# Kernel optimization log

Measured on AMD Instinct MI355X. Metric: run time of the kernel, lower is better.

The kernel has to match this reference:

```python
import jax, jax.numpy as jnp
import numpy as np

N_LEVELS = 16
F_PER_LEVEL = 2
LOG2_T = 19
TABLE_SIZE = 1 << LOG2_T
BASE_RES = 16.0
FINEST_RES = 512.0
# W == H == 512 -> x1 = y1 = 1.0
BOX_MIN = jnp.array([-1.0, -1.0], dtype=jnp.float32)
BOX_MAX = jnp.array([1.0, 1.0], dtype=jnp.float32)
# corner offsets, same order as torch BOX_OFFSETS: (0,0),(0,1),(1,0),(1,1)
OFFSETS = jnp.array([[i, j] for i in (0, 1) for j in (0, 1)], dtype=jnp.int32)
PRIME0 = jnp.uint32(1)
PRIME1 = jnp.uint32(2654435761)
HASH_MASK = jnp.uint32(TABLE_SIZE - 1)


def setup_inputs() -> dict:
    key = jax.random.key(0)
    ks = jax.random.split(key, 8)
    B, P = 4, 262144
    coord_2D = jax.random.uniform(ks[0], (B, P, 2), dtype=jnp.float32)  # in [0,1) subset of box
    embeddings = jax.random.normal(ks[1], (N_LEVELS, TABLE_SIZE, F_PER_LEVEL), dtype=jnp.float32)
    d_in = 2 + N_LEVELS * F_PER_LEVEL  # 34
    W0 = jax.random.normal(ks[2], (d_in, 256), dtype=jnp.float32) * 0.05
    b0 = jnp.zeros((256,), dtype=jnp.float32)
    W1 = jax.random.normal(ks[3], (256, 256), dtype=jnp.float32) * 0.05
    b1 = jnp.zeros((256,), dtype=jnp.float32)
    W2 = jax.random.normal(ks[4], (256, 3), dtype=jnp.float32) * 0.05
    b2 = jnp.zeros((3,), dtype=jnp.float32)
    return {"coord_2D": coord_2D, "embeddings": embeddings,
            "W0": W0, "b0": b0, "W1": W1, "b1": b1, "W2": W2, "b2": b2}


def _hash(corners_int32):
    # corners: [N,4,2] int32; xor of per-dim prime products, masked to table size (uint32 wraparound semantics)
    c = corners_int32.astype(jnp.uint32)
    h = (c[..., 0] * PRIME0) ^ (c[..., 1] * PRIME1)
    return (h & HASH_MASK).astype(jnp.int32)


def _encode(xy, embeddings):
    # xy: [N,2]; embeddings: [L, T, F]
    b = np.exp((np.log(FINEST_RES) - np.log(BASE_RES)) / (N_LEVELS - 1))
    resolutions = jnp.floor(BASE_RES * (b ** jnp.arange(N_LEVELS, dtype=jnp.float32)))  # [L]

    def level_encode(table, res):
        grid = (BOX_MAX - BOX_MIN) / res                     # [2]
        bl = jnp.floor((xy - BOX_MIN) / grid).astype(jnp.int32)  # bottom-left cell idx [N,2]
        vmin = bl.astype(xy.dtype) * grid + BOX_MIN          # voxel min vertex [N,2]
        w = (xy - vmin) / grid                               # bilinear weights [N,2]
        corners = bl[:, None, :] + OFFSETS                   # [N,4,2]
        emb = table[_hash(corners)]                          # gather: [N,4,F]
        wx = w[:, 0:1]
        wy = w[:, 1:2]
        c00 = emb[:, 0] * (1 - wx) + emb[:, 2] * wx
        c01 = emb[:, 1] * (1 - wx) + emb[:, 3] * wx
        return c00 * (1 - wy) + c01 * wy                     # [N,F]

    enc = jax.vmap(level_encode)(embeddings, resolutions)    # [L,N,F]
    return jnp.moveaxis(enc, 0, 1).reshape(xy.shape[0], N_LEVELS * F_PER_LEVEL)


def reference(coord_2D, embeddings, W0, b0, W1, b1, W2, b2):
    B = coord_2D.shape[0]
    xy = jnp.clip(coord_2D.reshape(-1, 2), BOX_MIN, BOX_MAX)
    enc = _encode(xy, embeddings)
    points_enc = jnp.concatenate([xy, enc], axis=-1)         # [N, 34]
    feat = jax.nn.relu(points_enc @ W0 + b0)
    feat = jax.nn.relu(feat @ W1 + b1)
    rgb = jax.nn.sigmoid(feat @ W2 + b2)
    return rgb.reshape(B, -1, 3)
```

## Files before the change

kernel.cpp:

```cpp
#include <hip/hip_runtime.h>
#include <hip/hip_bf16.h>
#include <cstdint>
#include <cstddef>

#define N_LEVELS   16
#define LOG2_T     19
#define TABLE_SIZE (1u << LOG2_T)
#define HASH_MASK  (TABLE_SIZE - 1u)
#define PRIME1     2654435761u

#define TPB 256
#define BT  64
#define FSTRIDE 72
#define HSTRIDE 264

typedef __attribute__((ext_vector_type(8))) short short8;
typedef __attribute__((ext_vector_type(4))) float floatx4;

__device__ __constant__ float c_res[N_LEVELS] = {
    16.f, 20.f, 25.f, 32.f, 40.f, 50.f, 64.f, 80.f,
    101.f, 128.f, 161.f, 203.f, 256.f, 322.f, 406.f, 512.f
};

__device__ __forceinline__ unsigned short f2bf(float x) {
    union { float f; uint32_t u; } v; v.f = x;
    const uint32_t u = v.u;
    return (unsigned short)((u + 0x7fffu + ((u >> 16) & 1u)) >> 16);
}

__device__ __forceinline__ uint32_t pk_bf16(float a, float b) {
#if __has_builtin(__builtin_amdgcn_cvt_pk_bf16_f32)
    typedef __attribute__((ext_vector_type(2))) __bf16 bf16x2;
    bf16x2 v = __builtin_amdgcn_cvt_pk_bf16_f32(a, b);
    uint32_t u; __builtin_memcpy(&u, &v, 4); return u;
#else
    return (uint32_t)f2bf(a) | ((uint32_t)f2bf(b) << 16);
#endif
}

__global__ void pack_weights(const float* __restrict__ W0,
                             const float* __restrict__ W1,
                             const float* __restrict__ W2,
                             unsigned short* __restrict__ ws)
{
    const int f = blockIdx.x;
    const int lane = threadIdx.x;
    const int q = lane >> 4, r = lane & 15;
    int layer, kt, nt;
    if (f < 32)       { layer = 0; kt = f >> 4;        nt = f & 15; }
    else if (f < 160) { layer = 1; kt = (f - 32) >> 4; nt = (f - 32) & 15; }
    else              { layer = 2; kt = f - 160;       nt = 0; }
    unsigned short vals[8];
    #pragma unroll
    for (int j = 0; j < 8; ++j) {
        const int k = kt * 32 + q * 8 + j;
        const int n = nt * 16 + r;
        float v = 0.f;
        if (layer == 0) {
            if (k < 32)       v = W0[(2 + k) * 256 + n];
            else if (k == 32) v = W0[0 * 256 + n];
            else if (k == 33) v = W0[1 * 256 + n];
        } else if (layer == 1) {
            v = W1[k * 256 + n];
        } else {
            if (n < 3) v = W2[k * 3 + n];
        }
        vals[j] = f2bf(v);
    }
    uint4 pk;
    pk.x = (uint32_t)vals[0] | ((uint32_t)vals[1] << 16);
    pk.y = (uint32_t)vals[2] | ((uint32_t)vals[3] << 16);
    pk.z = (uint32_t)vals[4] | ((uint32_t)vals[5] << 16);
    pk.w = (uint32_t)vals[6] | ((uint32_t)vals[7] << 16);
    *(uint4*)(ws + (size_t)f * 1024 + lane * 8) = pk;
}

__global__ __launch_bounds__(TPB, 2)
void fused_ngp_mlp(const float* __restrict__ coord,
                   const float* __restrict__ emb,
                   const unsigned short* __restrict__ wpack,
                   const float* __restrict__ b0,
                   const float* __restrict__ b1,
                   const float* __restrict__ b2,
                   float* __restrict__ out, int npoints)
{
    __shared__ unsigned short feat[BT][FSTRIDE];
    __shared__ unsigned short h[BT][HSTRIDE];

    const int t = threadIdx.x;
    const int p0 = blockIdx.x * BT;
    const int wave = t >> 6;
    const int lane = t & 63;
    const int q = lane >> 4, r = lane & 15;

    {
        const int p = t >> 2;
        const int k = t & 3;
        const int gp = p0 + p;
        float x = 0.f, y = 0.f;
        if (gp < npoints) {
            x = coord[2 * gp + 0]; y = coord[2 * gp + 1];
            x = fminf(fmaxf(x, -1.f), 1.f);
            y = fminf(fmaxf(y, -1.f), 1.f);
        }
        if (k == 0) {
            feat[p][32] = f2bf(x); feat[p][33] = f2bf(y);
            *(uint32_t*)&feat[p][34] = 0u;
            *(uint32_t*)&feat[p][36] = 0u;
            *(uint32_t*)&feat[p][38] = 0u;
        } else {
            const uint4 z = {0u, 0u, 0u, 0u};
            *(uint4*)&feat[p][40 + 8 * (k - 1)] = z;
        }
        #pragma unroll
        for (int i = 0; i < 4; ++i) {
            const int l = 4 * k + i;
            const float res  = c_res[l];
            const float grid = 2.0f / res;
            const float invg = res * 0.5f;
            const float tx = (x + 1.0f) / grid;
            const float ty = (y + 1.0f) / grid;
            const int bx = (int)floorf(tx);
            const int by = (int)floorf(ty);
            const float vx = (float)bx * grid - 1.0f;
            const float vy = (float)by * grid - 1.0f;
            const float wx = (x - vx) * invg;
            const float wy = (y - vy) * invg;
            const float2* tab = (const float2*)emb + (size_t)l * TABLE_SIZE;
            const uint32_t ux0 = (uint32_t)bx, ux1 = (uint32_t)(bx + 1);
            const uint32_t hy0 = (uint32_t)by * PRIME1;
            const uint32_t hy1 = (uint32_t)(by + 1) * PRIME1;
            const float2 e00 = tab[(ux0 ^ hy0) & HASH_MASK];
            const float2 e01 = tab[(ux0 ^ hy1) & HASH_MASK];
            const float2 e10 = tab[(ux1 ^ hy0) & HASH_MASK];
            const float2 e11 = tab[(ux1 ^ hy1) & HASH_MASK];
            const float owx = 1.f - wx, owy = 1.f - wy;
            const float f0 = (e00.x * owx + e10.x * wx) * owy + (e01.x * owx + e11.x * wx) * wy;
            const float f1 = (e00.y * owx + e10.y * wx) * owy + (e01.y * owx + e11.y * wx) * wy;
            *(uint32_t*)&feat[p][8 * k + 2 * i] = pk_bf16(f0, f1);
        }
    }
    __syncthreads();

    const unsigned short* w0p = wpack;
    const unsigned short* w1p = wpack + 32 * 1024;
    const unsigned short* w2p = wpack + 160 * 1024;

    {
        floatx4 acc[4][4];
        #pragma unroll
        for (int mti = 0; mti < 4; ++mti)
            #pragma unroll
            for (int nt = 0; nt < 4; ++nt)
                acc[mti][nt] = floatx4{0.f, 0.f, 0.f, 0.f};
        #pragma unroll
        for (int kt = 0; kt < 2; ++kt) {
            short8 a[4], b[4];
            #pragma unroll
            for (int mti = 0; mti < 4; ++mti)
                a[mti] = *(const short8*)(w0p + (size_t)(kt * 16 + wave * 4 + mti) * 1024 + lane * 8);
            #pragma unroll
            for (int nt = 0; nt < 4; ++nt)
                b[nt] = *(const short8*)&feat[16 * nt + r][kt * 32 + q * 8];
            #pragma unroll
            for (int mti = 0; mti < 4; ++mti)
                #pragma unroll
                for (int nt = 0; nt < 4; ++nt)
                    acc[mti][nt] = __builtin_amdgcn_mfma_f32_16x16x32_bf16(a[mti], b[nt], acc[mti][nt], 0, 0, 0);
        }
        #pragma unroll
        for (int mti = 0; mti < 4; ++mti) {
            const int col = (wave * 4 + mti) * 16 + 4 * q;
            const float4 bias = *(const float4*)&b0[col];
            #pragma unroll
            for (int nt = 0; nt < 4; ++nt) {
                const floatx4 a = acc[mti][nt];
                uint2 v;
                v.x = pk_bf16(fmaxf(a[0] + bias.x, 0.f), fmaxf(a[1] + bias.y, 0.f));
                v.y = pk_bf16(fmaxf(a[2] + bias.z, 0.f), fmaxf(a[3] + bias.w, 0.f));
                *(uint2*)&h[16 * nt + r][col] = v;
            }
        }
    }
    __syncthreads();

    {
        floatx4 acc[4][4];
        #pragma unroll
        for (int mti = 0; mti < 4; ++mti)
            #pragma unroll
            for (int nt = 0; nt < 4; ++nt)
                acc[mti][nt] = floatx4{0.f, 0.f, 0.f, 0.f};
        #pragma unroll 2
        for (int kt = 0; kt < 8; ++kt) {
            short8 a[4], b[4];
            #pragma unroll
            for (int mti = 0; mti < 4; ++mti)
                a[mti] = *(const short8*)(w1p + (size_t)(kt * 16 + wave * 4 + mti) * 1024 + lane * 8);
            #pragma unroll
            for (int nt = 0; nt < 4; ++nt)
                b[nt] = *(const short8*)&h[16 * nt + r][kt * 32 + q * 8];
            #pragma unroll
            for (int mti = 0; mti < 4; ++mti)
                #pragma unroll
                for (int nt = 0; nt < 4; ++nt)
                    acc[mti][nt] = __builtin_amdgcn_mfma_f32_16x16x32_bf16(a[mti], b[nt], acc[mti][nt], 0, 0, 0);
        }
        __syncthreads();
        #pragma unroll
        for (int mti = 0; mti < 4; ++mti) {
            const int col = (wave * 4 + mti) * 16 + 4 * q;
            const float4 bias = *(const float4*)&b1[col];
            #pragma unroll
            for (int nt = 0; nt < 4; ++nt) {
                const floatx4 a = acc[mti][nt];
                uint2 v;
                v.x = pk_bf16(fmaxf(a[0] + bias.x, 0.f), fmaxf(a[1] + bias.y, 0.f));
                v.y = pk_bf16(fmaxf(a[2] + bias.z, 0.f), fmaxf(a[3] + bias.w, 0.f));
                *(uint2*)&h[16 * nt + r][col] = v;
            }
        }
    }
    __syncthreads();

    {
        floatx4 acc = floatx4{0.f, 0.f, 0.f, 0.f};
        #pragma unroll
        for (int kt = 0; kt < 8; ++kt) {
            const short8 a = *(const short8*)(w2p + (size_t)kt * 1024 + lane * 8);
            const short8 b = *(const short8*)&h[16 * wave + r][kt * 32 + q * 8];
            acc = __builtin_amdgcn_mfma_f32_16x16x32_bf16(a, b, acc, 0, 0, 0);
        }
        if (q == 0) {
            const int gp = p0 + 16 * wave + r;
            if (gp < npoints) {
                #pragma unroll
                for (int reg = 0; reg < 3; ++reg) {
                    const float s = acc[reg] + b2[reg];
                    out[(size_t)gp * 3 + reg] = 1.f / (1.f + expf(-s));
                }
            }
        }
    }
}

extern "C" void kernel_launch(void* const* d_in, const int* in_sizes, int n_in,
                              void* d_out, int out_size, void* d_ws, size_t ws_size,
                              hipStream_t stream) {
    const float* coord = (const float*)d_in[0];
    const float* emb   = (const float*)d_in[1];
    const float* W0    = (const float*)d_in[2];
    const float* b0    = (const float*)d_in[3];
    const float* W1    = (const float*)d_in[4];
    const float* b1    = (const float*)d_in[5];
    const float* W2    = (const float*)d_in[6];
    const float* b2    = (const float*)d_in[7];
    float* out = (float*)d_out;
    unsigned short* ws = (unsigned short*)d_ws;

    const int npoints = in_sizes[0] / 2;
    const int blocks  = (npoints + BT - 1) / BT;

    hipLaunchKernelGGL(pack_weights, dim3(168), dim3(64), 0, stream, W0, W1, W2, ws);
    hipLaunchKernelGGL(fused_ngp_mlp, dim3(blocks), dim3(TPB), 0, stream,
                       coord, emb, ws, b0, b1, b2, out, npoints);
}
```

Baseline: 378.7 us.

## Split hash-grid encoding and MLP into separate kernels via workspace buffer

Replaces the single fused encode+MLP kernel with an encode kernel that writes bf16 features per point to global workspace, followed by an MLP kernel that reads them directly as MFMA B operands. This lets each kernel run with higher occupancy (launch bounds 4 instead of 2) and drops the shared-memory feature staging, so the latency-bound gathers and the MFMA work no longer compete for the same block. In exchange it adds a global round-trip of about 80 bytes per point plus an extra kernel launch. The fused kernel is kept as a fallback when the workspace is too small.

```diff
diff --git a/kernel.cpp b/kernel.cpp
--- a/kernel.cpp
+++ b/kernel.cpp
@@ -11,6 +11,7 @@
 
 #define TPB 256
 #define BT  64
+#define FROW 40
 #define FSTRIDE 72
 #define HSTRIDE 264
 
@@ -75,6 +76,191 @@
     *(uint4*)(ws + (size_t)f * 1024 + lane * 8) = pk;
 }
 
+__global__ __launch_bounds__(TPB, 4)
+void encode_kernel(const float* __restrict__ coord,
+                   const float* __restrict__ emb,
+                   unsigned short* __restrict__ featG, int npoints)
+{
+    const int gp = blockIdx.x * TPB + threadIdx.x;
+    if (gp >= npoints) return;
+    float x = coord[2 * gp + 0];
+    float y = coord[2 * gp + 1];
+    x = fminf(fmaxf(x, -1.f), 1.f);
+    y = fminf(fmaxf(y, -1.f), 1.f);
+
+    uint32_t e[N_LEVELS];
+    #pragma unroll
+    for (int l = 0; l < N_LEVELS; ++l) {
+        const float res  = c_res[l];
+        const float grid = 2.0f / res;
+        const float invg = res * 0.5f;
+        const float tx = (x + 1.0f) / grid;
+        const float ty = (y + 1.0f) / grid;
+        const int bx = (int)floorf(tx);
+        const int by = (int)floorf(ty);
+        const float vx = (float)bx * grid - 1.0f;
+        const float vy = (float)by * grid - 1.0f;
+        const float wx = (x - vx) * invg;
+        const float wy = (y - vy) * invg;
+        const float2* tab = (const float2*)emb + (size_t)l * TABLE_SIZE;
+        const uint32_t ux0 = (uint32_t)bx, ux1 = (uint32_t)(bx + 1);
+        const uint32_t hy0 = (uint32_t)by * PRIME1;
+        const uint32_t hy1 = (uint32_t)(by + 1) * PRIME1;
+        const float2 e00 = tab[(ux0 ^ hy0) & HASH_MASK];
+        const float2 e01 = tab[(ux0 ^ hy1) & HASH_MASK];
+        const float2 e10 = tab[(ux1 ^ hy0) & HASH_MASK];
+        const float2 e11 = tab[(ux1 ^ hy1) & HASH_MASK];
+        const float owx = 1.f - wx, owy = 1.f - wy;
+        const float f0 = (e00.x * owx + e10.x * wx) * owy + (e01.x * owx + e11.x * wx) * wy;
+        const float f1 = (e00.y * owx + e10.y * wx) * owy + (e01.y * owx + e11.y * wx) * wy;
+        e[l] = pk_bf16(f0, f1);
+    }
+
+    unsigned short* row = featG + (size_t)gp * FROW;
+    uint4 v;
+    v.x = e[0];  v.y = e[1];  v.z = e[2];  v.w = e[3];  *(uint4*)(row +  0) = v;
+    v.x = e[4];  v.y = e[5];  v.z = e[6];  v.w = e[7];  *(uint4*)(row +  8) = v;
+    v.x = e[8];  v.y = e[9];  v.z = e[10]; v.w = e[11]; *(uint4*)(row + 16) = v;
+    v.x = e[12]; v.y = e[13]; v.z = e[14]; v.w = e[15]; *(uint4*)(row + 24) = v;
+    v.x = pk_bf16(x, y); v.y = 0u; v.z = 0u; v.w = 0u;  *(uint4*)(row + 32) = v;
+}
+
+__global__ __launch_bounds__(TPB, 4)
+void mlp_kernel(const unsigned short* __restrict__ featG,
+                const unsigned short* __restrict__ wpack,
+                const float* __restrict__ b0,
+                const float* __restrict__ b1,
+                const float* __restrict__ b2,
+                float* __restrict__ out, int npoints)
+{
+    __shared__ unsigned short h[BT][HSTRIDE];
+
+    const int t = threadIdx.x;
+    const int p0 = blockIdx.x * BT;
+    const int wave = t >> 6;
+    const int lane = t & 63;
+    const int q = lane >> 4, r = lane & 15;
+
+    const unsigned short* w0p = wpack;
+    const unsigned short* w1p = wpack + 32 * 1024;
+    const unsigned short* w2p = wpack + 160 * 1024;
+
+    {
+        floatx4 acc[4][4];
+        #pragma unroll
+        for (int mti = 0; mti < 4; ++mti)
+            #pragma unroll
+            for (int nt = 0; nt < 4; ++nt)
+                acc[mti][nt] = floatx4{0.f, 0.f, 0.f, 0.f};
+
+        short8 a[4], b[4];
+        #pragma unroll
+        for (int mti = 0; mti < 4; ++mti)
+            a[mti] = *(const short8*)(w0p + (size_t)(0 * 16 + wave * 4 + mti) * 1024 + lane * 8);
+        #pragma unroll
+        for (int nt = 0; nt < 4; ++nt) {
+            const int row = min(p0 + 16 * nt + r, npoints - 1);
+            b[nt] = *(const short8*)(featG + (size_t)row * FROW + q * 8);
+        }
+        #pragma unroll
+        for (int mti = 0; mti < 4; ++mti)
+            #pragma unroll
+            for (int nt = 0; nt < 4; ++nt)
+                acc[mti][nt] = __builtin_amdgcn_mfma_f32_16x16x32_bf16(a[mti], b[nt], acc[mti][nt], 0, 0, 0);
+        #pragma unroll
+        for (int mti = 0; mti < 4; ++mti)
+            a[mti] = *(const short8*)(w0p + (size_t)(1 * 16 + wave * 4 + mti) * 1024 + lane * 8);
+        #pragma unroll
+        for (int nt = 0; nt < 4; ++nt) {
+            if (q == 0) {
+                const int row = min(p0 + 16 * nt + r, npoints - 1);
+                b[nt] = *(const short8*)(featG + (size_t)row * FROW + 32);
+            } else {
+                b[nt] = short8{0,0,0,0,0,0,0,0};
+            }
+        }
+        #pragma unroll
+        for (int mti = 0; mti < 4; ++mti)
+            #pragma unroll
+            for (int nt = 0; nt < 4; ++nt)
+                acc[mti][nt] = __builtin_amdgcn_mfma_f32_16x16x32_bf16(a[mti], b[nt], acc[mti][nt], 0, 0, 0);
+
+        #pragma unroll
+        for (int mti = 0; mti < 4; ++mti) {
+            const int col = (wave * 4 + mti) * 16 + 4 * q;
+            const float4 bias = *(const float4*)&b0[col];
+            #pragma unroll
+            for (int nt = 0; nt < 4; ++nt) {
+                const floatx4 a4 = acc[mti][nt];
+                uint2 v;
+                v.x = pk_bf16(fmaxf(a4[0] + bias.x, 0.f), fmaxf(a4[1] + bias.y, 0.f));
+                v.y = pk_bf16(fmaxf(a4[2] + bias.z, 0.f), fmaxf(a4[3] + bias.w, 0.f));
+                *(uint2*)&h[16 * nt + r][col] = v;
+            }
+        }
+    }
+    __syncthreads();
+
+    {
+        floatx4 acc[4][4];
+        #pragma unroll
+        for (int mti = 0; mti < 4; ++mti)
+            #pragma unroll
+            for (int nt = 0; nt < 4; ++nt)
+                acc[mti][nt] = floatx4{0.f, 0.f, 0.f, 0.f};
+        #pragma unroll 2
+        for (int kt = 0; kt < 8; ++kt) {
+            short8 a[4], b[4];
+            #pragma unroll
+            for (int mti = 0; mti < 4; ++mti)
+                a[mti] = *(const short8*)(w1p + (size_t)(kt * 16 + wave * 4 + mti) * 1024 + lane * 8);
+            #pragma unroll
+            for (int nt = 0; nt < 4; ++nt)
+                b[nt] = *(const short8*)&h[16 * nt + r][kt * 32 + q * 8];
+            #pragma unroll
+            for (int mti = 0; mti < 4; ++mti)
+                #pragma unroll
+                for (int nt = 0; nt < 4; ++nt)
+                    acc[mti][nt] = __builtin_amdgcn_mfma_f32_16x16x32_bf16(a[mti], b[nt], acc[mti][nt], 0, 0, 0);
+        }
+        __syncthreads();
+        #pragma unroll
+        for (int mti = 0; mti < 4; ++mti) {
+            const int col = (wave * 4 + mti) * 16 + 4 * q;
+            const float4 bias = *(const float4*)&b1[col];
+            #pragma unroll
+            for (int nt = 0; nt < 4; ++nt) {
+                const floatx4 a4 = acc[mti][nt];
+                uint2 v;
+                v.x = pk_bf16(fmaxf(a4[0] + bias.x, 0.f), fmaxf(a4[1] + bias.y, 0.f));
+                v.y = pk_bf16(fmaxf(a4[2] + bias.z, 0.f), fmaxf(a4[3] + bias.w, 0.f));
+                *(uint2*)&h[16 * nt + r][col] = v;
+            }
+        }
+    }
+    __syncthreads();
+
+    {
+        floatx4 acc = floatx4{0.f, 0.f, 0.f, 0.f};
+        #pragma unroll
+        for (int kt = 0; kt < 8; ++kt) {
+            const short8 a = *(const short8*)(w2p + (size_t)kt * 1024 + lane * 8);
+            const short8 b = *(const short8*)&h[16 * wave + r][kt * 32 + q * 8];
+            acc = __builtin_amdgcn_mfma_f32_16x16x32_bf16(a, b, acc, 0, 0, 0);
+        }
+        if (q == 0) {
+            const int gp = p0 + 16 * wave + r;
+            if (gp < npoints) {
+                #pragma unroll
+                for (int reg = 0; reg < 3; ++reg) {
+                    const float s = acc[reg] + b2[reg];
+                    out[(size_t)gp * 3 + reg] = 1.f / (1.f + expf(-s));
+                }
+            }
+        }
+    }
+}
+
 __global__ __launch_bounds__(TPB, 2)
 void fused_ngp_mlp(const float* __restrict__ coord,
                    const float* __restrict__ emb,
@@ -174,10 +360,10 @@
             const float4 bias = *(const float4*)&b0[col];
             #pragma unroll
             for (int nt = 0; nt < 4; ++nt) {
-                const floatx4 a = acc[mti][nt];
+                const floatx4 a4 = acc[mti][nt];
                 uint2 v;
-                v.x = pk_bf16(fmaxf(a[0] + bias.x, 0.f), fmaxf(a[1] + bias.y, 0.f));
-                v.y = pk_bf16(fmaxf(a[2] + bias.z, 0.f), fmaxf(a[3] + bias.w, 0.f));
+                v.x = pk_bf16(fmaxf(a4[0] + bias.x, 0.f), fmaxf(a4[1] + bias.y, 0.f));
+                v.y = pk_bf16(fmaxf(a4[2] + bias.z, 0.f), fmaxf(a4[3] + bias.w, 0.f));
                 *(uint2*)&h[16 * nt + r][col] = v;
             }
         }
@@ -213,10 +399,10 @@
             const float4 bias = *(const float4*)&b1[col];
             #pragma unroll
             for (int nt = 0; nt < 4; ++nt) {
-                const floatx4 a = acc[mti][nt];
+                const floatx4 a4 = acc[mti][nt];
                 uint2 v;
-                v.x = pk_bf16(fmaxf(a[0] + bias.x, 0.f), fmaxf(a[1] + bias.y, 0.f));
-                v.y = pk_bf16(fmaxf(a[2] + bias.z, 0.f), fmaxf(a[3] + bias.w, 0.f));
+                v.x = pk_bf16(fmaxf(a4[0] + bias.x, 0.f), fmaxf(a4[1] + bias.y, 0.f));
+                v.y = pk_bf16(fmaxf(a4[2] + bias.z, 0.f), fmaxf(a4[3] + bias.w, 0.f));
                 *(uint2*)&h[16 * nt + r][col] = v;
             }
         }
@@ -259,9 +445,22 @@
     unsigned short* ws = (unsigned short*)d_ws;
 
     const int npoints = in_sizes[0] / 2;
-    const int blocks  = (npoints + BT - 1) / BT;
+    const int mlp_blocks = (npoints + BT - 1) / BT;
+
+    const size_t pack_ushorts = 168u * 1024u;
+    const size_t need_bytes = (pack_ushorts + (size_t)npoints * FROW) * sizeof(unsigned short);
 
     hipLaunchKernelGGL(pack_weights, dim3(168), dim3(64), 0, stream, W0, W1, W2, ws);
-    hipLaunchKernelGGL(fused_ngp_mlp, dim3(blocks), dim3(TPB), 0, stream,
-                       coord, emb, ws, b0, b1, b2, out, npoints);
-}
+
+    if (ws_size >= need_bytes) {
+        unsigned short* featG = ws + pack_ushorts;
+        const int enc_blocks = (npoints + TPB - 1) / TPB;
+        hipLaunchKernelGGL(encode_kernel, dim3(enc_blocks), dim3(TPB), 0, stream,
+                           coord, emb, featG, npoints);
+        hipLaunchKernelGGL(mlp_kernel, dim3(mlp_blocks), dim3(TPB), 0, stream,
+                           featG, ws, b0, b1, b2, out, npoints);
+    } else {
+        hipLaunchKernelGGL(fused_ngp_mlp, dim3(mlp_blocks), dim3(TPB), 0, stream,
+                           coord, emb, ws, b0, b1, b2, out, npoints);
+    }
+}
```

Result: slower. 396.1 us (+4.6%).
